# Kernel tuning notes

Measured on AMD Instinct MI355X. Metric: run time of the kernel, lower is better.

The kernel has to match this reference:

```python
import jax, jax.numpy as jnp
import numpy as np

EMBED_DIM = 256
MAX_SENT_NUM = 50


def position_embeddings(max_sent_num, embed_dim):
    # pos[p, i] = sin(p / 200**(i/embed_dim))
    p = jnp.arange(max_sent_num, dtype=jnp.float32)[:, None]
    i = jnp.arange(embed_dim, dtype=jnp.float32)[None, :] / embed_dim
    return jnp.sin(p / jnp.power(200.0, i))


def setup_inputs() -> dict:
    key = jax.random.key(0)
    k1, k2, k3, k4 = jax.random.split(key, 4)
    B, S, N, E = 8192, 50, 20, EMBED_DIM
    return {
        "encoded_sents": jax.random.normal(k1, (B, S, E), dtype=jnp.float32),
        "entities": jax.random.normal(k2, (B, N, E), dtype=jnp.float32),
        "attn_matrix": jax.random.normal(k3, (E, E), dtype=jnp.float32) * 0.05,
        "dense_w": jax.random.normal(k4, (E, 1), dtype=jnp.float32) * 0.05,
        "dense_b": jnp.zeros((1,), dtype=jnp.float32),
    }


def reference(encoded_sents, entities, attn_matrix, dense_w, dense_b):
    B, S, E = encoded_sents.shape
    pos = position_embeddings(MAX_SENT_NUM, E)[:S]          # [S, E]
    x = encoded_sents + pos[None, :, :]                      # [B, S, E]

    # attention over previous sentences; query = last sentence's hidden state
    query = x[:, -1, :]                                      # [B, E]
    logits = jnp.einsum("be,bse->bs", query, x)              # [B, S]
    coef = jax.nn.softmax(logits, axis=1)                    # [B, S]
    attn_hidden = jnp.einsum("bs,bse->be", coef, x)          # [B, E]

    # entity attention: (query @ W) elementwise-weighted sum over entities (no softmax)
    q_ent = attn_hidden @ attn_matrix                        # [B, E]
    attn_ent = jnp.einsum("be,bne->be", q_ent, entities)     # [B, E] (sum over n)

    return jax.nn.sigmoid(attn_ent @ dense_w + dense_b)      # [B, 1]
```

## Files before the change

kernel.cpp:

```cpp
#include <hip/hip_runtime.h>
#include <math.h>

#define BATCH 8192
#define SENTS 50
#define ED    256
#define NENT  20
#define BB    16
#define NB    4

#define RATE_K 0.0298588132413075f

struct LoadSet {
    float4 xv[13];
    float4 qv;
    float4 ev[5];
};

__device__ __forceinline__ void issue_loads(
    LoadSet& S, const float* __restrict__ sents,
    const float* __restrict__ entities, int b, int r, int c, bool has13)
{
    const float4* s4 = (const float4*)(sents + (size_t)b * SENTS * ED);
    const float4* e4 = (const float4*)(entities + (size_t)b * NENT * ED);
    #pragma unroll
    for (int k = 0; k < 12; ++k) S.xv[k] = s4[(r + 4 * k) * 64 + c];
    S.qv = s4[49 * 64 + c];
    #pragma unroll
    for (int n = 0; n < 5; ++n) S.ev[n] = e4[(r + 4 * n) * 64 + c];
    if (has13) S.xv[12] = s4[(r + 48) * 64 + c];
}

__global__ __launch_bounds__(256) void attn_ent_kernel(
    const float* __restrict__ sents, const float* __restrict__ entities,
    const float* __restrict__ dense_w,
    float* __restrict__ h_out, float* __restrict__ m_out)
{
    __shared__ __align__(16) float hp[2][4][ED];
    __shared__ __align__(16) float ep[2][4][ED];
    __shared__ float md[2][4][2];

    int t  = threadIdx.x;
    int c  = t & 63;
    int r  = t >> 6;
    int b0 = blockIdx.x * NB;
    bool has13 = (r < 2);

    float4 rate;
    rate.x = exp2f(-(float)(4 * c + 0) * RATE_K);
    rate.y = exp2f(-(float)(4 * c + 1) * RATE_K);
    rate.z = exp2f(-(float)(4 * c + 2) * RATE_K);
    rate.w = exp2f(-(float)(4 * c + 3) * RATE_K);
    float wt = dense_w[t];

    LoadSet sA, sB;
    issue_loads(sA, sents, entities, b0, r, c, has13);

    #pragma unroll
    for (int j = 0; j < NB; ++j) {
        if (j + 1 < NB) {
            if ((j & 1) == 0) issue_loads(sB, sents, entities, b0 + j + 1, r, c, has13);
            else              issue_loads(sA, sents, entities, b0 + j + 1, r, c, has13);
        }
        LoadSet& S = ((j & 1) == 0) ? sA : sB;
        const int P = j & 1;
        const int b = b0 + j;

        float4 q;
        q.x = S.qv.x + __sinf(49.f * rate.x);
        q.y = S.qv.y + __sinf(49.f * rate.y);
        q.z = S.qv.z + __sinf(49.f * rate.z);
        q.w = S.qv.w + __sinf(49.f * rate.w);

        float4 x[13];
        float  lg[13];
        #pragma unroll
        for (int k = 0; k < 13; ++k) {
            if (k < 12 || has13) {
                float fs = (float)(r + 4 * k);
                x[k].x = S.xv[k].x + __sinf(fs * rate.x);
                x[k].y = S.xv[k].y + __sinf(fs * rate.y);
                x[k].z = S.xv[k].z + __sinf(fs * rate.z);
                x[k].w = S.xv[k].w + __sinf(fs * rate.w);
                float p = x[k].x * q.x + x[k].y * q.y + x[k].z * q.z + x[k].w * q.w;
                p += __shfl_xor(p, 1);
                p += __shfl_xor(p, 2);
                p += __shfl_xor(p, 4);
                p += __shfl_xor(p, 8);
                p += __shfl_xor(p, 16);
                p += __shfl_xor(p, 32);
                lg[k] = p;
            }
        }

        float mr = lg[0];
        #pragma unroll
        for (int k = 1; k < 13; ++k)
            if (k < 12 || has13) mr = fmaxf(mr, lg[k]);

        float dr = 0.f;
        float4 hacc = make_float4(0.f, 0.f, 0.f, 0.f);
        #pragma unroll
        for (int k = 0; k < 13; ++k) {
            if (k < 12 || has13) {
                float w = __expf(lg[k] - mr);
                dr += w;
                hacc.x += w * x[k].x; hacc.y += w * x[k].y;
                hacc.z += w * x[k].z; hacc.w += w * x[k].w;
            }
        }

        float4 es;
        es.x = ((S.ev[0].x + S.ev[1].x) + (S.ev[2].x + S.ev[3].x)) + S.ev[4].x;
        es.y = ((S.ev[0].y + S.ev[1].y) + (S.ev[2].y + S.ev[3].y)) + S.ev[4].y;
        es.z = ((S.ev[0].z + S.ev[1].z) + (S.ev[2].z + S.ev[3].z)) + S.ev[4].z;
        es.w = ((S.ev[0].w + S.ev[1].w) + (S.ev[2].w + S.ev[3].w)) + S.ev[4].w;

        *(float4*)&hp[P][r][4 * c] = hacc;
        *(float4*)&ep[P][r][4 * c] = es;
        if (c == 0) { md[P][r][0] = mr; md[P][r][1] = dr; }

        asm volatile("s_waitcnt lgkmcnt(0)" ::: "memory");
        __builtin_amdgcn_s_barrier();
        asm volatile("" ::: "memory");

        float m0 = md[P][0][0], d0 = md[P][0][1];
        float m1 = md[P][1][0], d1 = md[P][1][1];
        float m2 = md[P][2][0], d2 = md[P][2][1];
        float m3 = md[P][3][0], d3 = md[P][3][1];
        float M  = fmaxf(fmaxf(m0, m1), fmaxf(m2, m3));
        float s0 = __expf(m0 - M), s1 = __expf(m1 - M);
        float s2 = __expf(m2 - M), s3 = __expf(m3 - M);
        float dd = s0 * d0 + s1 * d1 + s2 * d2 + s3 * d3;
        float hv = s0 * hp[P][0][t] + s1 * hp[P][1][t]
                 + s2 * hp[P][2][t] + s3 * hp[P][3][t];
        h_out[(size_t)b * ED + t] = hv / dd;

        float ev = (ep[P][0][t] + ep[P][1][t]) + (ep[P][2][t] + ep[P][3][t]);
        m_out[(size_t)b * ED + t] = ev * wt;
    }
}

__global__ __launch_bounds__(256) void bilinear_kernel(
    const float* __restrict__ hws, const float* __restrict__ mws,
    const float* __restrict__ A, const float* __restrict__ dense_b,
    float* __restrict__ out)
{
    __shared__ __align__(16) float hl[BB][ED];
    __shared__ float ml[BB][ED];
    __shared__ float part[BB][ED];

    int t  = threadIdx.x;
    int b0 = blockIdx.x * BB;

    for (int i = 0; i < BB; ++i) {
        hl[i][t] = hws[(size_t)(b0 + i) * ED + t];
        ml[i][t] = mws[(size_t)(b0 + i) * ED + t];
    }
    __syncthreads();

    float acc[BB];
    #pragma unroll
    for (int i = 0; i < BB; ++i) acc[i] = 0.f;

    for (int ep = 0; ep < ED; ep += 4) {
        float a0 = A[(ep + 0) * ED + t];
        float a1 = A[(ep + 1) * ED + t];
        float a2 = A[(ep + 2) * ED + t];
        float a3 = A[(ep + 3) * ED + t];
        #pragma unroll
        for (int i = 0; i < BB; ++i) {
            float4 hv = *(const float4*)&hl[i][ep];
            acc[i] += hv.x * a0 + hv.y * a1 + hv.z * a2 + hv.w * a3;
        }
    }

    #pragma unroll
    for (int i = 0; i < BB; ++i) part[i][t] = acc[i] * ml[i][t];
    __syncthreads();

    int lane = t & 63, w = t >> 6;
    float bias = dense_b[0];
    for (int i = w; i < BB; i += 4) {
        float v = part[i][lane] + part[i][lane + 64] + part[i][lane + 128] + part[i][lane + 192];
        for (int off = 32; off >= 1; off >>= 1) v += __shfl_xor(v, off);
        if (lane == 0) out[b0 + i] = 1.f / (1.f + expf(-(v + bias)));
    }
}

__global__ __launch_bounds__(256) void fused_kernel(
    const float* __restrict__ sents, const float* __restrict__ entities,
    const float* __restrict__ A, const float* __restrict__ dense_w,
    const float* __restrict__ dense_b, float* __restrict__ out)
{
    __shared__ __align__(16) float xs[SENTS][ED + 4];
    __shared__ float logit_s[64];
    __shared__ float coef[64];
    __shared__ __align__(16) float harr[ED];
    __shared__ float marr[ED];
    __shared__ float red[4];

    int t    = threadIdx.x;
    int b    = blockIdx.x;
    int lane = t & 63;
    int w    = t >> 6;

    float rate = exp2f(-(float)t * RATE_K);
    const float* sp = sents + (size_t)b * SENTS * ED;
    for (int s = 0; s < SENTS; ++s)
        xs[s][t] = sp[s * ED + t] + sinf((float)s * rate);
    __syncthreads();

    float4 q = *(const float4*)&xs[SENTS - 1][lane * 4];
    for (int s = w; s < SENTS; s += 4) {
        float4 v = *(const float4*)&xs[s][lane * 4];
        float p = v.x * q.x + v.y * q.y + v.z * q.z + v.w * q.w;
        p += __shfl_down(p, 32);
        p += __shfl_down(p, 16);
        p += __shfl_down(p, 8);
        p += __shfl_down(p, 4);
        p += __shfl_down(p, 2);
        p += __shfl_down(p, 1);
        if (lane == 0) logit_s[s] = p;
    }
    __syncthreads();

    if (w == 0) {
        float l = (lane < SENTS) ? logit_s[lane] : -INFINITY;
        float mx = l;
        for (int off = 32; off >= 1; off >>= 1) mx = fmaxf(mx, __shfl_xor(mx, off));
        float ex = (lane < SENTS) ? expf(l - mx) : 0.f;
        float sm = ex;
        for (int off = 32; off >= 1; off >>= 1) sm += __shfl_xor(sm, off);
        if (lane < SENTS) coef[lane] = ex / sm;
    }
    __syncthreads();

    float h = 0.f;
    #pragma unroll
    for (int s = 0; s < SENTS; ++s) h += coef[s] * xs[s][t];

    const float* ent = entities + (size_t)b * NENT * ED;
    float es = 0.f;
    #pragma unroll
    for (int n = 0; n < NENT; ++n) es += ent[n * ED + t];
    float m = es * dense_w[t];

    harr[t] = h;
    marr[t] = m;
    __syncthreads();

    float acc = 0.f;
    for (int ep = 0; ep < ED; ep += 4) {
        float4 hv = *(const float4*)&harr[ep];
        acc += hv.x * A[(ep + 0) * ED + t];
        acc += hv.y * A[(ep + 1) * ED + t];
        acc += hv.z * A[(ep + 2) * ED + t];
        acc += hv.w * A[(ep + 3) * ED + t];
    }
    float val = acc * marr[t];
    val += __shfl_down(val, 32);
    val += __shfl_down(val, 16);
    val += __shfl_down(val, 8);
    val += __shfl_down(val, 4);
    val += __shfl_down(val, 2);
    val += __shfl_down(val, 1);
    if (lane == 0) red[w] = val;
    __syncthreads();
    if (t == 0) {
        float tot = red[0] + red[1] + red[2] + red[3];
        out[b] = 1.f / (1.f + expf(-(tot + dense_b[0])));
    }
}

extern "C" void kernel_launch(void* const* d_in, const int* in_sizes, int n_in,
                              void* d_out, int out_size, void* d_ws, size_t ws_size,
                              hipStream_t stream) {
    const float* sents    = (const float*)d_in[0];
    const float* entities = (const float*)d_in[1];
    const float* A        = (const float*)d_in[2];
    const float* dense_w  = (const float*)d_in[3];
    const float* dense_b  = (const float*)d_in[4];
    float* out = (float*)d_out;

    size_t hm_bytes = (size_t)BATCH * ED * sizeof(float);
    size_t need = 2 * hm_bytes;

    if (ws_size >= need) {
        float* hws = (float*)d_ws;
        float* mws = (float*)((char*)d_ws + hm_bytes);
        attn_ent_kernel<<<BATCH / NB, 256, 0, stream>>>(sents, entities, dense_w, hws, mws);
        bilinear_kernel<<<BATCH / BB, 256, 0, stream>>>(hws, mws, A, dense_b, out);
    } else {
        fused_kernel<<<BATCH, 256, 0, stream>>>(sents, entities, A, dense_w, dense_b, out);
    }
}
```

Measured before the change: 154.3 us.

## Split sentence attention and entity sum into separate block roles with nontemporal loads

Replaces the four-batch-per-block software-pipelined kernel with one kernel whose blocks take one of two roles: one block per batch for sentence attention, and blocks that each sum entities for four batches. This drops the register double-buffering and makes the grid much larger, aiming for more memory parallelism from many small blocks instead of explicit prefetch. Streaming reads now use nontemporal loads, and the final sigmoid uses fast exp. The cost is less latency hiding inside each block and per-block setup (rate computation) that is repeated for every batch.

After: 132.8 us (median of 2 runs). 13.9% less time.

```diff
diff --git a/kernel.cpp b/kernel.cpp
--- a/kernel.cpp
+++ b/kernel.cpp
@@ -6,81 +6,61 @@
 #define ED    256
 #define NENT  20
 #define BB    16
-#define NB    4
+
+#define SENT_BLOCKS BATCH
+#define ENT_BLOCKS  (BATCH / 4)
 
 #define RATE_K 0.0298588132413075f
 
-struct LoadSet {
-    float4 xv[13];
-    float4 qv;
-    float4 ev[5];
-};
-
-__device__ __forceinline__ void issue_loads(
-    LoadSet& S, const float* __restrict__ sents,
-    const float* __restrict__ entities, int b, int r, int c, bool has13)
-{
-    const float4* s4 = (const float4*)(sents + (size_t)b * SENTS * ED);
-    const float4* e4 = (const float4*)(entities + (size_t)b * NENT * ED);
-    #pragma unroll
-    for (int k = 0; k < 12; ++k) S.xv[k] = s4[(r + 4 * k) * 64 + c];
-    S.qv = s4[49 * 64 + c];
-    #pragma unroll
-    for (int n = 0; n < 5; ++n) S.ev[n] = e4[(r + 4 * n) * 64 + c];
-    if (has13) S.xv[12] = s4[(r + 48) * 64 + c];
-}
-
-__global__ __launch_bounds__(256) void attn_ent_kernel(
+typedef float f4 __attribute__((ext_vector_type(4)));
+
+__global__ __launch_bounds__(256) void fat_kernel(
     const float* __restrict__ sents, const float* __restrict__ entities,
     const float* __restrict__ dense_w,
     float* __restrict__ h_out, float* __restrict__ m_out)
 {
-    __shared__ __align__(16) float hp[2][4][ED];
-    __shared__ __align__(16) float ep[2][4][ED];
-    __shared__ float md[2][4][2];
-
-    int t  = threadIdx.x;
-    int c  = t & 63;
-    int r  = t >> 6;
-    int b0 = blockIdx.x * NB;
-    bool has13 = (r < 2);
-
-    float4 rate;
-    rate.x = exp2f(-(float)(4 * c + 0) * RATE_K);
-    rate.y = exp2f(-(float)(4 * c + 1) * RATE_K);
-    rate.z = exp2f(-(float)(4 * c + 2) * RATE_K);
-    rate.w = exp2f(-(float)(4 * c + 3) * RATE_K);
-    float wt = dense_w[t];
-
-    LoadSet sA, sB;
-    issue_loads(sA, sents, entities, b0, r, c, has13);
-
-    #pragma unroll
-    for (int j = 0; j < NB; ++j) {
-        if (j + 1 < NB) {
-            if ((j & 1) == 0) issue_loads(sB, sents, entities, b0 + j + 1, r, c, has13);
-            else              issue_loads(sA, sents, entities, b0 + j + 1, r, c, has13);
-        }
-        LoadSet& S = ((j & 1) == 0) ? sA : sB;
-        const int P = j & 1;
-        const int b = b0 + j;
-
-        float4 q;
-        q.x = S.qv.x + __sinf(49.f * rate.x);
-        q.y = S.qv.y + __sinf(49.f * rate.y);
-        q.z = S.qv.z + __sinf(49.f * rate.z);
-        q.w = S.qv.w + __sinf(49.f * rate.w);
-
-        float4 x[13];
-        float  lg[13];
+    __shared__ __align__(16) float hp[4][ED];
+    __shared__ float md[4][2];
+
+    int t = threadIdx.x;
+
+    if (blockIdx.x < SENT_BLOCKS) {
+        int b = blockIdx.x;
+        int c = t & 63;
+        int r = t >> 6;
+        bool has13 = (r < 2);
+
+        const f4* s4 = (const f4*)(sents + (size_t)b * SENTS * ED);
+
+        f4 qv = __builtin_nontemporal_load(&s4[49 * 64 + c]);
+        f4 xv[13];
+        #pragma unroll
+        for (int k = 0; k < 12; ++k)
+            xv[k] = __builtin_nontemporal_load(&s4[(r + 4 * k) * 64 + c]);
+        if (has13) xv[12] = __builtin_nontemporal_load(&s4[(r + 48) * 64 + c]);
+
+        f4 rate;
+        rate.x = exp2f(-(float)(4 * c + 0) * RATE_K);
+        rate.y = exp2f(-(float)(4 * c + 1) * RATE_K);
+        rate.z = exp2f(-(float)(4 * c + 2) * RATE_K);
+        rate.w = exp2f(-(float)(4 * c + 3) * RATE_K);
+
+        f4 q;
+        q.x = qv.x + __sinf(49.f * rate.x);
+        q.y = qv.y + __sinf(49.f * rate.y);
+        q.z = qv.z + __sinf(49.f * rate.z);
+        q.w = qv.w + __sinf(49.f * rate.w);
+
+        f4 x[13];
+        float lg[13];
         #pragma unroll
         for (int k = 0; k < 13; ++k) {
             if (k < 12 || has13) {
                 float fs = (float)(r + 4 * k);
-                x[k].x = S.xv[k].x + __sinf(fs * rate.x);
-                x[k].y = S.xv[k].y + __sinf(fs * rate.y);
-                x[k].z = S.xv[k].z + __sinf(fs * rate.z);
-                x[k].w = S.xv[k].w + __sinf(fs * rate.w);
+                x[k].x = xv[k].x + __sinf(fs * rate.x);
+                x[k].y = xv[k].y + __sinf(fs * rate.y);
+                x[k].z = xv[k].z + __sinf(fs * rate.z);
+                x[k].w = xv[k].w + __sinf(fs * rate.w);
                 float p = x[k].x * q.x + x[k].y * q.y + x[k].z * q.z + x[k].w * q.w;
                 p += __shfl_xor(p, 1);
                 p += __shfl_xor(p, 2);
@@ -98,7 +78,7 @@
             if (k < 12 || has13) mr = fmaxf(mr, lg[k]);
 
         float dr = 0.f;
-        float4 hacc = make_float4(0.f, 0.f, 0.f, 0.f);
+        f4 hacc = (f4)0.f;
         #pragma unroll
         for (int k = 0; k < 13; ++k) {
             if (k < 12 || has13) {
@@ -109,34 +89,38 @@
             }
         }
 
-        float4 es;
-        es.x = ((S.ev[0].x + S.ev[1].x) + (S.ev[2].x + S.ev[3].x)) + S.ev[4].x;
-        es.y = ((S.ev[0].y + S.ev[1].y) + (S.ev[2].y + S.ev[3].y)) + S.ev[4].y;
-        es.z = ((S.ev[0].z + S.ev[1].z) + (S.ev[2].z + S.ev[3].z)) + S.ev[4].z;
-        es.w = ((S.ev[0].w + S.ev[1].w) + (S.ev[2].w + S.ev[3].w)) + S.ev[4].w;
-
-        *(float4*)&hp[P][r][4 * c] = hacc;
-        *(float4*)&ep[P][r][4 * c] = es;
-        if (c == 0) { md[P][r][0] = mr; md[P][r][1] = dr; }
-
-        asm volatile("s_waitcnt lgkmcnt(0)" ::: "memory");
-        __builtin_amdgcn_s_barrier();
-        asm volatile("" ::: "memory");
-
-        float m0 = md[P][0][0], d0 = md[P][0][1];
-        float m1 = md[P][1][0], d1 = md[P][1][1];
-        float m2 = md[P][2][0], d2 = md[P][2][1];
-        float m3 = md[P][3][0], d3 = md[P][3][1];
+        *(f4*)&hp[r][4 * c] = hacc;
+        if (c == 0) { md[r][0] = mr; md[r][1] = dr; }
+        __syncthreads();
+
+        float m0 = md[0][0], d0 = md[0][1];
+        float m1 = md[1][0], d1 = md[1][1];
+        float m2 = md[2][0], d2 = md[2][1];
+        float m3 = md[3][0], d3 = md[3][1];
         float M  = fmaxf(fmaxf(m0, m1), fmaxf(m2, m3));
         float s0 = __expf(m0 - M), s1 = __expf(m1 - M);
         float s2 = __expf(m2 - M), s3 = __expf(m3 - M);
         float dd = s0 * d0 + s1 * d1 + s2 * d2 + s3 * d3;
-        float hv = s0 * hp[P][0][t] + s1 * hp[P][1][t]
-                 + s2 * hp[P][2][t] + s3 * hp[P][3][t];
+        float hv = s0 * hp[0][t] + s1 * hp[1][t] + s2 * hp[2][t] + s3 * hp[3][t];
         h_out[(size_t)b * ED + t] = hv / dd;
-
-        float ev = (ep[P][0][t] + ep[P][1][t]) + (ep[P][2][t] + ep[P][3][t]);
-        m_out[(size_t)b * ED + t] = ev * wt;
+    } else {
+        int b = (blockIdx.x - SENT_BLOCKS) * 4 + (t >> 6);
+        int c = t & 63;
+
+        const f4* e4 = (const f4*)(entities + (size_t)b * NENT * ED);
+
+        f4 a[NENT];
+        #pragma unroll
+        for (int n = 0; n < NENT; ++n)
+            a[n] = __builtin_nontemporal_load(&e4[n * 64 + c]);
+
+        f4 s = (f4)0.f;
+        #pragma unroll
+        for (int n = 0; n < NENT; ++n) s += a[n];
+
+        f4 w4 = ((const f4*)dense_w)[c];
+        s *= w4;
+        ((f4*)(m_out + (size_t)b * ED))[c] = s;
     }
 }
 
@@ -183,7 +167,7 @@
     for (int i = w; i < BB; i += 4) {
         float v = part[i][lane] + part[i][lane + 64] + part[i][lane + 128] + part[i][lane + 192];
         for (int off = 32; off >= 1; off >>= 1) v += __shfl_xor(v, off);
-        if (lane == 0) out[b0 + i] = 1.f / (1.f + expf(-(v + bias)));
+        if (lane == 0) out[b0 + i] = 1.f / (1.f + __expf(-(v + bias)));
     }
 }
 
@@ -288,7 +272,8 @@
     if (ws_size >= need) {
         float* hws = (float*)d_ws;
         float* mws = (float*)((char*)d_ws + hm_bytes);
-        attn_ent_kernel<<<BATCH / NB, 256, 0, stream>>>(sents, entities, dense_w, hws, mws);
+        fat_kernel<<<SENT_BLOCKS + ENT_BLOCKS, 256, 0, stream>>>(
+            sents, entities, dense_w, hws, mws);
         bilinear_kernel<<<BATCH / BB, 256, 0, stream>>>(hws, mws, A, dense_b, out);
     } else {
         fused_kernel<<<BATCH, 256, 0, stream>>>(sents, entities, A, dense_w, dense_b, out);
```
